# Kernel tuning notes

Measured on AMD Instinct MI355X. Metric: run time of the kernel, lower is better.

The kernel has to match this reference:

```python
import jax, jax.numpy as jnp
import numpy as np

N = 50000
E = 800000
NEG_SLOPE = 0.2
BN_EPS = 1e-5


def _gat_conv(x, src, dst, W, a_src, a_dst, bias, heads, out_ch, concat):
    # Linear projection per head: [N, heads, out_ch]
    h = (x @ W).reshape(-1, heads, out_ch)
    # Per-node attention terms alpha_src/alpha_dst: [N, heads]
    al_s = (h * a_src[None]).sum(-1)
    al_d = (h * a_dst[None]).sum(-1)
    # Edge logits with LeakyReLU: [E, heads]
    logits = jax.nn.leaky_relu(al_s[src] + al_d[dst], NEG_SLOPE)
    # Segment (scatter) softmax over edges grouped by destination node
    m = jax.ops.segment_max(logits, dst, num_segments=N)
    e = jnp.exp(logits - m[dst])
    s = jax.ops.segment_sum(e, dst, num_segments=N)
    alpha = e / (s[dst] + 1e-16)                      # [E, heads]
    # Weighted message aggregation: scatter-add to destinations
    msg = h[src] * alpha[:, :, None]                  # [E, heads, out_ch]
    out = jax.ops.segment_sum(msg, dst, num_segments=N)  # [N, heads, out_ch]
    out = out.reshape(-1, heads * out_ch) if concat else out.mean(axis=1)
    return out + bias


def _bn_eval(x, gamma, beta, mean, var):
    return (x - mean) * jax.lax.rsqrt(var + BN_EPS) * gamma + beta


def setup_inputs() -> dict:
    key = jax.random.key(0)
    ks = jax.random.split(key, 12)
    in_ch, hid, heads, out_cls = 128, 64, 2, 40
    return {
        "x": jax.random.normal(ks[0], (N, in_ch), jnp.float32),
        "edge_index": jax.random.randint(ks[1], (2, E), 0, N, jnp.int32),
        "W1": jax.random.normal(ks[2], (in_ch, heads * hid), jnp.float32) * 0.1,
        "a1_src": jax.random.normal(ks[3], (heads, hid), jnp.float32) * 0.1,
        "a1_dst": jax.random.normal(ks[4], (heads, hid), jnp.float32) * 0.1,
        "b1": jnp.zeros((heads * hid,), jnp.float32),
        "bn1_gamma": jnp.ones((heads * hid,), jnp.float32),
        "bn1_beta": jnp.zeros((heads * hid,), jnp.float32),
        "bn1_mean": jax.random.normal(ks[5], (heads * hid,), jnp.float32) * 0.1,
        "bn1_var": jax.random.uniform(ks[6], (heads * hid,), jnp.float32, 0.5, 1.5),
        "W2": jax.random.normal(ks[7], (heads * hid, out_cls), jnp.float32) * 0.1,
        "a2_src": jax.random.normal(ks[8], (1, out_cls), jnp.float32) * 0.1,
        "a2_dst": jax.random.normal(ks[9], (1, out_cls), jnp.float32) * 0.1,
        "b2": jnp.zeros((out_cls,), jnp.float32),
    }


def reference(x, edge_index, W1, a1_src, a1_dst, b1, bn1_gamma, bn1_beta,
              bn1_mean, bn1_var, W2, a2_src, a2_dst, b2):
    # add self loops
    loops = jnp.arange(N, dtype=edge_index.dtype)
    src = jnp.concatenate([edge_index[0], loops])
    dst = jnp.concatenate([edge_index[1], loops])
    # layer 1: GATConv(heads=2, concat) -> BN(eval) -> ReLU (dropout is eval no-op)
    h = _gat_conv(x, src, dst, W1, a1_src, a1_dst, b1, heads=2, out_ch=64, concat=True)
    h = jax.nn.relu(_bn_eval(h, bn1_gamma, bn1_beta, bn1_mean, bn1_var))
    # output layer: GATConv(heads=1, concat=False)
    out = _gat_conv(h, src, dst, W2, a2_src, a2_dst, b2, heads=1, out_ch=40, concat=False)
    return jax.nn.log_softmax(out, axis=1)
```

## Files before the change

### kernel.cpp

```cpp
#include <hip/hip_runtime.h>
#include <hip/hip_bf16.h>

#define NEG_SLOPE 0.2f
#define BN_EPS 1e-5f

#define NBLK 256
#define COARSE_SHIFT 9
#define COARSE_NPB 512

__device__ __forceinline__ float wred_sum(float v) {
    #pragma unroll
    for (int m = 32; m > 0; m >>= 1) v += __shfl_xor(v, m);
    return v;
}
__device__ __forceinline__ float wred_max(float v) {
    #pragma unroll
    for (int m = 32; m > 0; m >>= 1) v = fmaxf(v, __shfl_xor(v, m));
    return v;
}
__device__ __forceinline__ int wred_isum(int v) {
    #pragma unroll
    for (int m = 32; m > 0; m >>= 1) v += __shfl_xor(v, m);
    return v;
}
__device__ __forceinline__ float xor16_sum(float v) {
    #pragma unroll
    for (int m = 1; m < 16; m <<= 1) v += __shfl_xor(v, m);
    return v;
}

__device__ __forceinline__ unsigned pack_bf16(float a, float b) {
    __hip_bfloat162 t;
    t.x = __float2bfloat16(a);
    t.y = __float2bfloat16(b);
    return *(unsigned*)&t;
}
__device__ __forceinline__ float2 unpack_bf16(unsigned u) {
    __hip_bfloat162 t = *(__hip_bfloat162*)&u;
    return {__bfloat162float(t.x), __bfloat162float(t.y)};
}

__device__ __forceinline__ unsigned enc_ord(float f) {
    unsigned u = __float_as_uint(f);
    return (u & 0x80000000u) ? ~u : (u | 0x80000000u);
}
__device__ __forceinline__ float dec_ord(unsigned e) {
    unsigned u = (e & 0x80000000u) ? (e ^ 0x80000000u) : ~e;
    return __uint_as_float(u);
}

__global__ __launch_bounds__(256) void part_hist(const int* __restrict__ ei, int E, int Et,
                                                 int chunk, int* __restrict__ hist, int nCoarse) {
    __shared__ int h[128];
    int b = blockIdx.x, t = threadIdx.x;
    if (t < 128) h[t] = 0;
    __syncthreads();
    int beg = b * chunk, end = min(beg + chunk, Et);
    for (int idx = beg + t; idx < end; idx += 256) {
        int d = (idx < E) ? ei[E + idx] : (idx - E);
        atomicAdd(&h[d >> COARSE_SHIFT], 1);
    }
    __syncthreads();
    if (t < nCoarse) hist[t * NBLK + b] = h[t];
}

__global__ __launch_bounds__(1024) void csr_mid(int* __restrict__ hist,
                                                int* __restrict__ cbase, int nCoarse) {
    __shared__ int ctot_s[128];
    __shared__ int scn[128];
    __shared__ int cb_s[129];
    int t = threadIdx.x;
    int wv = t >> 6, ln = t & 63;
    if (t < 128) ctot_s[t] = 0;
    __syncthreads();
    for (int c = wv; c < nCoarse; c += 16) {
        int idx = c * NBLK + 4 * ln;
        int4 v = *(int4*)&hist[idx];
        int s = wred_isum(v.x + v.y + v.z + v.w);
        if (ln == 0) ctot_s[c] = s;
    }
    __syncthreads();
    int v0 = 0;
    if (t < 128) { v0 = ctot_s[t]; scn[t] = v0; }
    __syncthreads();
    for (int off = 1; off < 128; off <<= 1) {
        int u = (t >= off && t < 128) ? scn[t - off] : 0;
        __syncthreads();
        if (t < 128) scn[t] += u;
        __syncthreads();
    }
    if (t < 128) cb_s[t] = scn[t] - v0;
    if (t == 127) cb_s[128] = scn[127];
    __syncthreads();
    if (t <= nCoarse) cbase[t] = cb_s[t];
    for (int c = wv; c < nCoarse; c += 16) {
        int base = cb_s[c];
        int idx = c * NBLK + 4 * ln;
        int4 v = *(int4*)&hist[idx];
        int sl = v.x + v.y + v.z + v.w;
        int inc = sl;
        #pragma unroll
        for (int off = 1; off < 64; off <<= 1) {
            int u = __shfl_up(inc, off);
            if (ln >= off) inc += u;
        }
        int exc = inc - sl + base;
        int4 o;
        o.x = exc;
        o.y = exc + v.x;
        o.z = exc + v.x + v.y;
        o.w = exc + v.x + v.y + v.z;
        *(int4*)&hist[idx] = o;
    }
}

__global__ __launch_bounds__(256) void part_scatter(const int* __restrict__ ei, int E, int Et,
                                                    int chunk, const int* __restrict__ hist,
                                                    unsigned* __restrict__ staged, int nCoarse) {
    __shared__ int cur[128];
    int b = blockIdx.x, t = threadIdx.x;
    if (t < nCoarse) cur[t] = hist[t * NBLK + b];
    __syncthreads();
    int beg = b * chunk, end = min(beg + chunk, Et);
    for (int idx = beg + t; idx < end; idx += 256) {
        int s, d;
        if (idx < E) { s = ei[idx]; d = ei[E + idx]; }
        else         { s = idx - E; d = idx - E; }
        int c = d >> COARSE_SHIFT;
        int pos = atomicAdd(&cur[c], 1);
        staged[pos] = ((unsigned)s << COARSE_SHIFT) | (unsigned)(d & (COARSE_NPB - 1));
    }
}

__global__ __launch_bounds__(512) void fine_place(const unsigned* __restrict__ staged,
                                                  const int* __restrict__ cbase,
                                                  int* __restrict__ offs,
                                                  int* __restrict__ csr, int Nn, int nCoarse) {
    __shared__ int hcnt[COARSE_NPB];
    __shared__ int scn[COARSE_NPB];
    int b = blockIdx.x, t = threadIdx.x;
    int node0 = b << COARSE_SHIFT;
    int nloc = min(COARSE_NPB, Nn - node0);
    hcnt[t] = 0;
    __syncthreads();
    int ebeg = cbase[b], eend = cbase[b + 1];
    for (int p = ebeg + t; p < eend; p += 512) {
        atomicAdd(&hcnt[staged[p] & (COARSE_NPB - 1)], 1);
    }
    __syncthreads();
    int val = hcnt[t];
    scn[t] = val;
    __syncthreads();
    for (int off = 1; off < COARSE_NPB; off <<= 1) {
        int u = (t >= off) ? scn[t - off] : 0;
        __syncthreads();
        scn[t] += u;
        __syncthreads();
    }
    int exc = ebeg + scn[t] - val;
    if (t < nloc) offs[node0 + t] = exc;
    if (b == nCoarse - 1 && t == 0) offs[Nn] = eend;
    hcnt[t] = exc;
    __syncthreads();
    for (int p = ebeg + t; p < eend; p += 512) {
        unsigned v = staged[p];
        int pos = atomicAdd(&hcnt[v & (COARSE_NPB - 1)], 1);
        csr[pos] = (int)(v >> COARSE_SHIFT);
    }
}

__global__ __launch_bounds__(256) void gemm1_tiled(const float* __restrict__ x,
                                                   const float* __restrict__ W,
                                                   const float* __restrict__ a1s,
                                                   const float* __restrict__ a1d,
                                                   unsigned* __restrict__ h1b,
                                                   float* __restrict__ als,
                                                   float* __restrict__ ald, int Nn) {
    __shared__ float Ast[32][132];
    __shared__ float Bs[32][132];
    int t  = threadIdx.x;
    int tx = t & 15;
    int ty = t >> 4;
    int br = blockIdx.x * 128;

    float acc[8][8];
    #pragma unroll
    for (int i = 0; i < 8; ++i)
        #pragma unroll
        for (int j = 0; j < 8; ++j) acc[i][j] = 0.f;

    int k4   = t & 7;
    int rowA = t >> 3;

    for (int k0 = 0; k0 < 128; k0 += 32) {
        #pragma unroll
        for (int i = 0; i < 4; ++i) {
            int r  = rowA + 32 * i;
            int gr = min(br + r, Nn - 1);
            float4 v = *(const float4*)(x + (size_t)gr * 128 + k0 + 4 * k4);
            Ast[4 * k4 + 0][r] = v.x; Ast[4 * k4 + 1][r] = v.y;
            Ast[4 * k4 + 2][r] = v.z; Ast[4 * k4 + 3][r] = v.w;
        }
        #pragma unroll
        for (int i = 0; i < 4; ++i) {
            int f  = t + 256 * i;
            int kk = f >> 5, c4 = f & 31;
            *(float4*)&Bs[kk][4 * c4] = *(const float4*)(W + (size_t)(k0 + kk) * 128 + 4 * c4);
        }
        __syncthreads();
        #pragma unroll 8
        for (int kk = 0; kk < 32; ++kk) {
            float4 a0 = *(const float4*)&Ast[kk][8 * ty];
            float4 a1 = *(const float4*)&Ast[kk][8 * ty + 4];
            float4 b0 = *(const float4*)&Bs[kk][8 * tx];
            float4 b1 = *(const float4*)&Bs[kk][8 * tx + 4];
            float av[8] = {a0.x, a0.y, a0.z, a0.w, a1.x, a1.y, a1.z, a1.w};
            float bv[8] = {b0.x, b0.y, b0.z, b0.w, b1.x, b1.y, b1.z, b1.w};
            #pragma unroll
            for (int i = 0; i < 8; ++i)
                #pragma unroll
                for (int j = 0; j < 8; ++j) acc[i][j] += av[i] * bv[j];
        }
        __syncthreads();
    }

    float a_s[8], a_d[8];
    #pragma unroll
    for (int j = 0; j < 8; ++j) { a_s[j] = a1s[8 * tx + j]; a_d[j] = a1d[8 * tx + j]; }
    bool h0 = (tx < 8);

    #pragma unroll
    for (int i = 0; i < 8; ++i) {
        int r = br + 8 * ty + i;
        if (r < Nn) {
            uint4 pk;
            pk.x = pack_bf16(acc[i][0], acc[i][1]);
            pk.y = pack_bf16(acc[i][2], acc[i][3]);
            pk.z = pack_bf16(acc[i][4], acc[i][5]);
            pk.w = pack_bf16(acc[i][6], acc[i][7]);
            *(uint4*)(h1b + (size_t)r * 64 + 4 * tx) = pk;
        }
        float ps = 0.f, pd = 0.f;
        #pragma unroll
        for (int j = 0; j < 8; ++j) { ps += acc[i][j] * a_s[j]; pd += acc[i][j] * a_d[j]; }
        float s0 = xor16_sum(h0 ? ps : 0.f);
        float s1 = xor16_sum(h0 ? 0.f : ps);
        float d0 = xor16_sum(h0 ? pd : 0.f);
        float d1 = xor16_sum(h0 ? 0.f : pd);
        if (tx == 0 && r < Nn) {
            als[r * 2] = s0; als[r * 2 + 1] = s1;
            ald[r * 2] = d0; ald[r * 2 + 1] = d1;
        }
    }
}

template <int H>
__global__ __launch_bounds__(256) void almax_kernel(const float* __restrict__ als,
                                                    unsigned* __restrict__ gmax, int off, int Nn,
                                                    const float* __restrict__ b1,
                                                    const float* __restrict__ g1,
                                                    const float* __restrict__ be1,
                                                    const float* __restrict__ mn1,
                                                    const float* __restrict__ vr1,
                                                    float* __restrict__ bnscale,
                                                    float* __restrict__ bnshift) {
    __shared__ float red[4][H];
    int t = threadIdx.x;
    if (bnscale && blockIdx.x == 0 && t < 128) {
        float sc = rsqrtf(vr1[t] + BN_EPS) * g1[t];
        bnscale[t] = sc;
        bnshift[t] = be1[t] + (b1[t] - mn1[t]) * sc;
    }
    float m[H];
    #pragma unroll
    for (int h = 0; h < H; ++h) m[h] = -1e30f;
    for (int n = blockIdx.x * 256 + t; n < Nn; n += gridDim.x * 256) {
        #pragma unroll
        for (int h = 0; h < H; ++h) m[h] = fmaxf(m[h], als[n * H + h]);
    }
    #pragma unroll
    for (int h = 0; h < H; ++h) m[h] = wred_max(m[h]);
    int wid = t >> 6;
    if ((t & 63) == 0) {
        #pragma unroll
        for (int h = 0; h < H; ++h) red[wid][h] = m[h];
    }
    __syncthreads();
    if (t == 0) {
        #pragma unroll
        for (int h = 0; h < H; ++h) {
            float mm = fmaxf(fmaxf(red[0][h], red[1][h]), fmaxf(red[2][h], red[3][h]));
            atomicMax(&gmax[off + h], enc_ord(mm));
        }
    }
}

__global__ __launch_bounds__(256) void softagg1_kernel(const int* __restrict__ offs, const int* __restrict__ csr,
                            const unsigned* __restrict__ h1b,
                            const float* __restrict__ als, const float* __restrict__ ald,
                            const unsigned* __restrict__ gmax,
                            const float* __restrict__ bnscale, const float* __restrict__ bnshift,
                            unsigned* __restrict__ hbnb, int Nn) {
    __shared__ int   sh_s[4][4][16];
    __shared__ float sh_e[4][4][2][16];
    int wid = threadIdx.x >> 6, lane = threadIdx.x & 63;
    int g = lane >> 4;
    int l = lane & 15;
    int head = l >> 3;
    int n = blockIdx.x * 16 + wid * 4 + g;
    if (n >= Nn) return;
    int b = offs[n], e = offs[n + 1];
    float2 aldn = *(const float2*)(ald + (size_t)n * 2);
    float bd0 = dec_ord(gmax[0]) + aldn.x; bd0 = (bd0 > 0.f) ? bd0 : NEG_SLOPE * bd0;
    float bd1 = dec_ord(gmax[1]) + aldn.y; bd1 = (bd1 > 0.f) ? bd1 : NEG_SLOPE * bd1;

    float acc[8];
    #pragma unroll
    for (int j = 0; j < 8; ++j) acc[j] = 0.f;
    float den0 = 0.f, den1 = 0.f;

    for (int base = b; base < e; base += 16) {
        int cnt = min(16, e - base);
        int   s1 = 0;
        float e0r = 0.f, e1r = 0.f;
        if (l < cnt) {
            s1 = csr[base + l];
            float2 as = *(const float2*)(als + (size_t)s1 * 2);
            float l0 = as.x + aldn.x; l0 = (l0 > 0.f) ? l0 : NEG_SLOPE * l0;
            float l1 = as.y + aldn.y; l1 = (l1 > 0.f) ? l1 : NEG_SLOPE * l1;
            e0r = __expf(l0 - bd0);
            e1r = __expf(l1 - bd1);
            den0 += e0r; den1 += e1r;
        }
        sh_s[wid][g][l]    = s1;
        sh_e[wid][g][0][l] = e0r;
        sh_e[wid][g][1][l] = e1r;
        int i = 0;
        for (; i + 1 < cnt; i += 2) {
            int   sA  = sh_s[wid][g][i];
            int   sB  = sh_s[wid][g][i + 1];
            float evA = sh_e[wid][g][head][i];
            float evB = sh_e[wid][g][head][i + 1];
            uint4 vA = *(const uint4*)(h1b + (size_t)sA * 64 + 4 * l);
            uint4 vB = *(const uint4*)(h1b + (size_t)sB * 64 + 4 * l);
            float2 f;
            f = unpack_bf16(vA.x); acc[0] += f.x * evA; acc[1] += f.y * evA;
            f = unpack_bf16(vA.y); acc[2] += f.x * evA; acc[3] += f.y * evA;
            f = unpack_bf16(vA.z); acc[4] += f.x * evA; acc[5] += f.y * evA;
            f = unpack_bf16(vA.w); acc[6] += f.x * evA; acc[7] += f.y * evA;
            f = unpack_bf16(vB.x); acc[0] += f.x * evB; acc[1] += f.y * evB;
            f = unpack_bf16(vB.y); acc[2] += f.x * evB; acc[3] += f.y * evB;
            f = unpack_bf16(vB.z); acc[4] += f.x * evB; acc[5] += f.y * evB;
            f = unpack_bf16(vB.w); acc[6] += f.x * evB; acc[7] += f.y * evB;
        }
        if (i < cnt) {
            int   s  = sh_s[wid][g][i];
            float ev = sh_e[wid][g][head][i];
            uint4 v = *(const uint4*)(h1b + (size_t)s * 64 + 4 * l);
            float2 f;
            f = unpack_bf16(v.x); acc[0] += f.x * ev; acc[1] += f.y * ev;
            f = unpack_bf16(v.y); acc[2] += f.x * ev; acc[3] += f.y * ev;
            f = unpack_bf16(v.z); acc[4] += f.x * ev; acc[5] += f.y * ev;
            f = unpack_bf16(v.w); acc[6] += f.x * ev; acc[7] += f.y * ev;
        }
    }
    #pragma unroll
    for (int m = 1; m < 16; m <<= 1) {
        den0 += __shfl_xor(den0, m);
        den1 += __shfl_xor(den1, m);
    }
    float inv = 1.f / ((head ? den1 : den0) + 1e-16f);
    int c = 8 * l;
    float4 sa = *(const float4*)(bnscale + c), sb = *(const float4*)(bnscale + c + 4);
    float4 ha = *(const float4*)(bnshift + c), hb = *(const float4*)(bnshift + c + 4);
    float o0 = fmaxf(acc[0] * inv * sa.x + ha.x, 0.f);
    float o1 = fmaxf(acc[1] * inv * sa.y + ha.y, 0.f);
    float o2 = fmaxf(acc[2] * inv * sa.z + ha.z, 0.f);
    float o3 = fmaxf(acc[3] * inv * sa.w + ha.w, 0.f);
    float o4 = fmaxf(acc[4] * inv * sb.x + hb.x, 0.f);
    float o5 = fmaxf(acc[5] * inv * sb.y + hb.y, 0.f);
    float o6 = fmaxf(acc[6] * inv * sb.z + hb.z, 0.f);
    float o7 = fmaxf(acc[7] * inv * sb.w + hb.w, 0.f);
    uint4 pk = {pack_bf16(o0, o1), pack_bf16(o2, o3), pack_bf16(o4, o5), pack_bf16(o6, o7)};
    *(uint4*)(hbnb + (size_t)n * 64 + 4 * l) = pk;
}

__global__ __launch_bounds__(256) void gemm2_tiled(const unsigned* __restrict__ hbnb,
                                                   const float* __restrict__ W2,
                                                   const float* __restrict__ a2s,
                                                   const float* __restrict__ a2d,
                                                   unsigned* __restrict__ h2b,
                                                   float* __restrict__ als, float* __restrict__ ald,
                                                   int Nn) {
    __shared__ float Ast[32][132];
    __shared__ float Bs[32][68];
    int t  = threadIdx.x;
    int tx = t & 15;
    int ty = t >> 4;
    int br = blockIdx.x * 128;

    float as4[4], ad4[4];
    #pragma unroll
    for (int j = 0; j < 4; ++j) {
        int c = 4 * tx + j;
        as4[j] = (c < 40) ? a2s[c] : 0.f;
        ad4[j] = (c < 40) ? a2d[c] : 0.f;
    }

    float acc[8][4];
    #pragma unroll
    for (int i = 0; i < 8; ++i)
        #pragma unroll
        for (int j = 0; j < 4; ++j) acc[i][j] = 0.f;

    int k4   = t & 7;
    int rowA = t >> 3;

    for (int k0 = 0; k0 < 128; k0 += 32) {
        #pragma unroll
        for (int i = 0; i < 4; ++i) {
            int r  = rowA + 32 * i;
            int gr = min(br + r, Nn - 1);
            uint2 v2 = *(const uint2*)(hbnb + (size_t)gr * 64 + (k0 >> 1) + 2 * k4);
            float2 f0 = unpack_bf16(v2.x), f1 = unpack_bf16(v2.y);
            Ast[4 * k4 + 0][r] = f0.x; Ast[4 * k4 + 1][r] = f0.y;
            Ast[4 * k4 + 2][r] = f1.x; Ast[4 * k4 + 3][r] = f1.y;
        }
        #pragma unroll
        for (int i = 0; i < 2; ++i) {
            int f  = t + 256 * i;
            int kk = f >> 4, c4 = f & 15;
            float4 v = {0.f, 0.f, 0.f, 0.f};
            if (c4 < 10) v = *(const float4*)(W2 + (size_t)(k0 + kk) * 40 + 4 * c4);
            *(float4*)&Bs[kk][4 * c4] = v;
        }
        __syncthreads();
        #pragma unroll 8
        for (int kk = 0; kk < 32; ++kk) {
            float4 a0 = *(const float4*)&Ast[kk][8 * ty];
            float4 a1 = *(const float4*)&Ast[kk][8 * ty + 4];
            float4 b0 = *(const float4*)&Bs[kk][4 * tx];
            float av[8] = {a0.x, a0.y, a0.z, a0.w, a1.x, a1.y, a1.z, a1.w};
            #pragma unroll
            for (int i = 0; i < 8; ++i) {
                acc[i][0] += av[i] * b0.x; acc[i][1] += av[i] * b0.y;
                acc[i][2] += av[i] * b0.z; acc[i][3] += av[i] * b0.w;
            }
        }
        __syncthreads();
    }

    #pragma unroll
    for (int i = 0; i < 8; ++i) {
        int r = br + 8 * ty + i;
        if (r < Nn && tx < 10) {
            uint2 pk = {pack_bf16(acc[i][0], acc[i][1]), pack_bf16(acc[i][2], acc[i][3])};
            *(uint2*)(h2b + (size_t)r * 20 + 2 * tx) = pk;
        }
        float ps = acc[i][0] * as4[0] + acc[i][1] * as4[1] + acc[i][2] * as4[2] + acc[i][3] * as4[3];
        float pd = acc[i][0] * ad4[0] + acc[i][1] * ad4[1] + acc[i][2] * ad4[2] + acc[i][3] * ad4[3];
        float sS = xor16_sum(ps);
        float sD = xor16_sum(pd);
        if (tx == 0 && r < Nn) { als[r] = sS; ald[r] = sD; }
    }
}

__global__ __launch_bounds__(256) void softagg2_kernel(const int* __restrict__ offs, const int* __restrict__ csr,
                            const unsigned* __restrict__ h2b,
                            const float* __restrict__ als, const float* __restrict__ ald,
                            const unsigned* __restrict__ gmax,
                            const float* __restrict__ b2,
                            float* __restrict__ out, int Nn) {
    __shared__ int   sh_s[4][8][8];
    __shared__ float sh_ev[4][8][8];
    int wid = threadIdx.x >> 6, lane = threadIdx.x & 63;
    int g = lane >> 3;
    int l = lane & 7;
    int n = blockIdx.x * 32 + wid * 8 + g;
    if (n >= Nn) return;
    int b = offs[n], e = offs[n + 1];
    float aldn = ald[n];
    float bound = dec_ord(gmax[2]) + aldn;
    bound = (bound > 0.f) ? bound : NEG_SLOPE * bound;

    float acc[8];
    #pragma unroll
    for (int j = 0; j < 8; ++j) acc[j] = 0.f;
    float den = 0.f;

    for (int base = b; base < e; base += 8) {
        int cnt = min(8, e - base);
        int   s1 = 0;
        float evr = 0.f;
        if (l < cnt) {
            s1 = csr[base + l];
            float lv = als[s1] + aldn;
            lv = (lv > 0.f) ? lv : NEG_SLOPE * lv;
            evr = __expf(lv - bound);
            den += evr;
        }
        sh_s[wid][g][l]  = s1;
        sh_ev[wid][g][l] = evr;
        if (l < 5) {
            int i = 0;
            for (; i + 1 < cnt; i += 2) {
                int   sA  = sh_s[wid][g][i];
                int   sB  = sh_s[wid][g][i + 1];
                float evA = sh_ev[wid][g][i];
                float evB = sh_ev[wid][g][i + 1];
                uint4 vA = *(const uint4*)(h2b + (size_t)sA * 20 + 4 * l);
                uint4 vB = *(const uint4*)(h2b + (size_t)sB * 20 + 4 * l);
                float2 f;
                f = unpack_bf16(vA.x); acc[0] += f.x * evA; acc[1] += f.y * evA;
                f = unpack_bf16(vA.y); acc[2] += f.x * evA; acc[3] += f.y * evA;
                f = unpack_bf16(vA.z); acc[4] += f.x * evA; acc[5] += f.y * evA;
                f = unpack_bf16(vA.w); acc[6] += f.x * evA; acc[7] += f.y * evA;
                f = unpack_bf16(vB.x); acc[0] += f.x * evB; acc[1] += f.y * evB;
                f = unpack_bf16(vB.y); acc[2] += f.x * evB; acc[3] += f.y * evB;
                f = unpack_bf16(vB.z); acc[4] += f.x * evB; acc[5] += f.y * evB;
                f = unpack_bf16(vB.w); acc[6] += f.x * evB; acc[7] += f.y * evB;
            }
            if (i < cnt) {
                int   s  = sh_s[wid][g][i];
                float ev = sh_ev[wid][g][i];
                uint4 v = *(const uint4*)(h2b + (size_t)s * 20 + 4 * l);
                float2 f;
                f = unpack_bf16(v.x); acc[0] += f.x * ev; acc[1] += f.y * ev;
                f = unpack_bf16(v.y); acc[2] += f.x * ev; acc[3] += f.y * ev;
                f = unpack_bf16(v.z); acc[4] += f.x * ev; acc[5] += f.y * ev;
                f = unpack_bf16(v.w); acc[6] += f.x * ev; acc[7] += f.y * ev;
            }
        }
    }
    #pragma unroll
    for (int m = 1; m < 8; m <<= 1) den += __shfl_xor(den, m);
    float inv = 1.f / (den + 1e-16f);
    bool valid = (l < 5);
    float vv[8];
    float lmax = -1e30f;
    if (valid) {
        int c = 8 * l;
        #pragma unroll
        for (int j = 0; j < 8; ++j) {
            vv[j] = acc[j] * inv + b2[c + j];
            lmax = fmaxf(lmax, vv[j]);
        }
    }
    float m = lmax;
    #pragma unroll
    for (int mm = 1; mm < 8; mm <<= 1) m = fmaxf(m, __shfl_xor(m, mm));
    float es = 0.f;
    if (valid) {
        #pragma unroll
        for (int j = 0; j < 8; ++j) es += __expf(vv[j] - m);
    }
    #pragma unroll
    for (int mm = 1; mm < 8; mm <<= 1) es += __shfl_xor(es, mm);
    float lse = m + logf(es);
    if (valid) {
        float4 oa = {vv[0] - lse, vv[1] - lse, vv[2] - lse, vv[3] - lse};
        float4 ob = {vv[4] - lse, vv[5] - lse, vv[6] - lse, vv[7] - lse};
        *(float4*)(out + (size_t)n * 40 + 8 * l)     = oa;
        *(float4*)(out + (size_t)n * 40 + 8 * l + 4) = ob;
    }
}

extern "C" void kernel_launch(void* const* d_in, const int* in_sizes, int n_in,
                              void* d_out, int out_size, void* d_ws, size_t ws_size,
                              hipStream_t stream) {
    const float* x    = (const float*)d_in[0];
    const int*   ei   = (const int*)d_in[1];
    const float* W1   = (const float*)d_in[2];
    const float* a1s  = (const float*)d_in[3];
    const float* a1d  = (const float*)d_in[4];
    const float* b1   = (const float*)d_in[5];
    const float* g1   = (const float*)d_in[6];
    const float* be1  = (const float*)d_in[7];
    const float* mn1  = (const float*)d_in[8];
    const float* vr1  = (const float*)d_in[9];
    const float* W2   = (const float*)d_in[10];
    const float* a2s  = (const float*)d_in[11];
    const float* a2d  = (const float*)d_in[12];
    const float* b2   = (const float*)d_in[13];
    float* out = (float*)d_out;

    const int N  = in_sizes[0] / 128;
    const int E  = in_sizes[1] / 2;
    const int Et = E + N;
    const int nCoarse = (N + COARSE_NPB - 1) >> COARSE_SHIFT;
    const int chunk   = (Et + NBLK - 1) / NBLK;

    char* p = (char*)d_ws;
    auto alloc = [&](size_t bytes) -> void* {
        void* r = (void*)p;
        p += (bytes + 255) & ~(size_t)255;
        return r;
    };
    int*      hist   = (int*)alloc((size_t)nCoarse * NBLK * 4);
    int*      cbase  = (int*)alloc((size_t)(nCoarse + 1) * 4);
    int*      offs   = (int*)alloc((size_t)(N + 1) * 4);
    unsigned* staged = (unsigned*)alloc((size_t)Et * 4);
    int*      csr    = (int*)alloc((size_t)Et * 4);
    unsigned* h1b    = (unsigned*)alloc((size_t)N * 64 * 4);
    float*    al1sv  = (float*)alloc((size_t)N * 2 * 4);
    float*    al1dv  = (float*)alloc((size_t)N * 2 * 4);
    unsigned* hbnb   = (unsigned*)alloc((size_t)N * 64 * 4);
    unsigned* h2b    = (unsigned*)alloc((size_t)N * 20 * 4);
    float*    al2sv  = (float*)alloc((size_t)N * 4);
    float*    al2dv  = (float*)alloc((size_t)N * 4);
    unsigned* gmax   = (unsigned*)alloc(4 * 4);
    float*    bnscale= (float*)alloc(128 * 4);
    float*    bnshift= (float*)alloc(128 * 4);
    (void)ws_size;

    hipMemsetAsync(gmax, 0, 16, stream);

    part_hist<<<NBLK, 256, 0, stream>>>(ei, E, Et, chunk, hist, nCoarse);
    csr_mid<<<1, 1024, 0, stream>>>(hist, cbase, nCoarse);
    part_scatter<<<NBLK, 256, 0, stream>>>(ei, E, Et, chunk, hist, staged, nCoarse);
    fine_place<<<nCoarse, 512, 0, stream>>>(staged, cbase, offs, csr, N, nCoarse);

    gemm1_tiled<<<(N + 127) / 128, 256, 0, stream>>>(x, W1, a1s, a1d, h1b, al1sv, al1dv, N);
    almax_kernel<2><<<64, 256, 0, stream>>>(al1sv, gmax, 0, N, b1, g1, be1, mn1, vr1, bnscale, bnshift);
    softagg1_kernel<<<(N + 15) / 16, 256, 0, stream>>>(offs, csr, h1b, al1sv, al1dv, gmax,
                                                       bnscale, bnshift, hbnb, N);

    gemm2_tiled<<<(N + 127) / 128, 256, 0, stream>>>(hbnb, W2, a2s, a2d, h2b, al2sv, al2dv, N);
    almax_kernel<1><<<64, 256, 0, stream>>>(al2sv, gmax, 2, N, nullptr, nullptr, nullptr, nullptr,
                                            nullptr, nullptr, nullptr);
    softagg2_kernel<<<(N + 31) / 32, 256, 0, stream>>>(offs, csr, h2b, al2sv, al2dv, gmax, b2, out, N);
}
```

Before: 241.3 us.

## Use bf16 MFMA for first-layer projection GEMM and fold gmax reset into histogram

Replaces the FP32 register-tiled SIMT GEMM for layer 1 with a bf16 MFMA 16x16x32 kernel. W is converted into per-lane bf16 fragments in shared memory, x rows are converted to bf16 on load, and accumulators are staged through LDS so h1 is written as packed bf16 rows. It also removes the separate memset launch by zeroing gmax inside part_hist. Inputs to the projection now lose precision to bf16, and each block re-gathers and converts all of W with uncoalesced loads.

```diff
diff --git a/kernel.cpp b/kernel.cpp
--- a/kernel.cpp
+++ b/kernel.cpp
@@ -7,6 +7,9 @@
 #define NBLK 256
 #define COARSE_SHIFT 9
 #define COARSE_NPB 512
+
+typedef __attribute__((ext_vector_type(8))) short s8v;
+typedef __attribute__((ext_vector_type(4))) float f4v;
 
 __device__ __forceinline__ float wred_sum(float v) {
     #pragma unroll
@@ -39,6 +42,10 @@
     __hip_bfloat162 t = *(__hip_bfloat162*)&u;
     return {__bfloat162float(t.x), __bfloat162float(t.y)};
 }
+__device__ __forceinline__ short bf16s(float f) {
+    __hip_bfloat16 h = __float2bfloat16(f);
+    return *(short*)&h;
+}
 
 __device__ __forceinline__ unsigned enc_ord(float f) {
     unsigned u = __float_as_uint(f);
@@ -50,9 +57,11 @@
 }
 
 __global__ __launch_bounds__(256) void part_hist(const int* __restrict__ ei, int E, int Et,
-                                                 int chunk, int* __restrict__ hist, int nCoarse) {
+                                                 int chunk, int* __restrict__ hist, int nCoarse,
+                                                 unsigned* __restrict__ gmax) {
     __shared__ int h[128];
     int b = blockIdx.x, t = threadIdx.x;
+    if (b == 0 && t < 4) gmax[t] = 0u;
     if (t < 128) h[t] = 0;
     __syncthreads();
     int beg = b * chunk, end = min(beg + chunk, Et);
@@ -169,87 +178,103 @@
     }
 }
 
-__global__ __launch_bounds__(256) void gemm1_tiled(const float* __restrict__ x,
-                                                   const float* __restrict__ W,
-                                                   const float* __restrict__ a1s,
-                                                   const float* __restrict__ a1d,
-                                                   unsigned* __restrict__ h1b,
-                                                   float* __restrict__ als,
-                                                   float* __restrict__ ald, int Nn) {
-    __shared__ float Ast[32][132];
-    __shared__ float Bs[32][132];
-    int t  = threadIdx.x;
-    int tx = t & 15;
-    int ty = t >> 4;
-    int br = blockIdx.x * 128;
-
-    float acc[8][8];
-    #pragma unroll
-    for (int i = 0; i < 8; ++i)
-        #pragma unroll
-        for (int j = 0; j < 8; ++j) acc[i][j] = 0.f;
-
-    int k4   = t & 7;
-    int rowA = t >> 3;
-
-    for (int k0 = 0; k0 < 128; k0 += 32) {
+__global__ __launch_bounds__(256) void gemm1_mfma(const float* __restrict__ x,
+                                                  const float* __restrict__ W,
+                                                  const float* __restrict__ a1s,
+                                                  const float* __restrict__ a1d,
+                                                  unsigned* __restrict__ h1b,
+                                                  float* __restrict__ als,
+                                                  float* __restrict__ ald, int Nn) {
+    __shared__ __align__(16) char smem[33792];
+    short* fragtab = (short*)smem;
+    float* lout    = (float*)smem;
+
+    int t = threadIdx.x;
+    int br = blockIdx.x * 64;
+
+    #pragma unroll
+    for (int i = 0; i < 8; ++i) {
+        int s   = t + 256 * i;
+        int grp = s >> 6;
+        int ls  = s & 63;
+        int ct = grp >> 2, kc = grp & 3;
+        int nn = ls & 15, quad = ls >> 4;
+        int kb = kc * 32 + quad * 8;
+        int cc = ct * 16 + nn;
+        #pragma unroll
+        for (int j = 0; j < 8; ++j)
+            fragtab[s * 8 + j] = bf16s(W[(size_t)(kb + j) * 128 + cc]);
+    }
+    __syncthreads();
+
+    int w    = t >> 6;
+    int lane = t & 63;
+    int nn   = lane & 15;
+    int quad = lane >> 4;
+    int rowbase = br + w * 16;
+    int arow = min(rowbase + nn, Nn - 1);
+    const float* xr = x + (size_t)arow * 128;
+
+    f4v acc[8];
+    #pragma unroll
+    for (int ct = 0; ct < 8; ++ct) acc[ct] = (f4v){0.f, 0.f, 0.f, 0.f};
+
+    #pragma unroll
+    for (int kc = 0; kc < 4; ++kc) {
+        float4 v0 = *(const float4*)(xr + kc * 32 + quad * 8);
+        float4 v1 = *(const float4*)(xr + kc * 32 + quad * 8 + 4);
+        union { s8v s; uint4 u; } A;
+        A.u.x = pack_bf16(v0.x, v0.y); A.u.y = pack_bf16(v0.z, v0.w);
+        A.u.z = pack_bf16(v1.x, v1.y); A.u.w = pack_bf16(v1.z, v1.w);
+        #pragma unroll
+        for (int ct = 0; ct < 8; ++ct) {
+            s8v B = *(s8v*)(fragtab + (size_t)((ct * 4 + kc) * 64 + lane) * 8);
+            acc[ct] = __builtin_amdgcn_mfma_f32_16x16x32_bf16(A.s, B, acc[ct], 0, 0, 0);
+        }
+    }
+
+    float s_c[8], d_c[8];
+    #pragma unroll
+    for (int ct = 0; ct < 8; ++ct) {
+        s_c[ct] = a1s[ct * 16 + nn];
+        d_c[ct] = a1d[ct * 16 + nn];
+    }
+    #pragma unroll
+    for (int reg = 0; reg < 4; ++reg) {
+        float ps0 = 0.f, pd0 = 0.f, ps1 = 0.f, pd1 = 0.f;
+        #pragma unroll
+        for (int ct = 0; ct < 4; ++ct) { ps0 += acc[ct][reg] * s_c[ct]; pd0 += acc[ct][reg] * d_c[ct]; }
+        #pragma unroll
+        for (int ct = 4; ct < 8; ++ct) { ps1 += acc[ct][reg] * s_c[ct]; pd1 += acc[ct][reg] * d_c[ct]; }
+        ps0 = xor16_sum(ps0); pd0 = xor16_sum(pd0);
+        ps1 = xor16_sum(ps1); pd1 = xor16_sum(pd1);
+        int r = rowbase + quad * 4 + reg;
+        if (nn == 0 && r < Nn) {
+            als[(size_t)r * 2]     = ps0;
+            als[(size_t)r * 2 + 1] = ps1;
+            ald[(size_t)r * 2]     = pd0;
+            ald[(size_t)r * 2 + 1] = pd1;
+        }
+    }
+
+    __syncthreads();
+    #pragma unroll
+    for (int ct = 0; ct < 8; ++ct)
+        #pragma unroll
+        for (int reg = 0; reg < 4; ++reg)
+            lout[w * 2112 + (quad * 4 + reg) * 132 + ct * 16 + nn] = acc[ct][reg];
+    int row_l = lane >> 2;
+    int ch    = lane & 3;
+    int r = rowbase + row_l;
+    if (r < Nn) {
+        const float* src = lout + w * 2112 + row_l * 132 + ch * 32;
         #pragma unroll
         for (int i = 0; i < 4; ++i) {
-            int r  = rowA + 32 * i;
-            int gr = min(br + r, Nn - 1);
-            float4 v = *(const float4*)(x + (size_t)gr * 128 + k0 + 4 * k4);
-            Ast[4 * k4 + 0][r] = v.x; Ast[4 * k4 + 1][r] = v.y;
-            Ast[4 * k4 + 2][r] = v.z; Ast[4 * k4 + 3][r] = v.w;
-        }
-        #pragma unroll
-        for (int i = 0; i < 4; ++i) {
-            int f  = t + 256 * i;
-            int kk = f >> 5, c4 = f & 31;
-            *(float4*)&Bs[kk][4 * c4] = *(const float4*)(W + (size_t)(k0 + kk) * 128 + 4 * c4);
-        }
-        __syncthreads();
-        #pragma unroll 8
-        for (int kk = 0; kk < 32; ++kk) {
-            float4 a0 = *(const float4*)&Ast[kk][8 * ty];
-            float4 a1 = *(const float4*)&Ast[kk][8 * ty + 4];
-            float4 b0 = *(const float4*)&Bs[kk][8 * tx];
-            float4 b1 = *(const float4*)&Bs[kk][8 * tx + 4];
-            float av[8] = {a0.x, a0.y, a0.z, a0.w, a1.x, a1.y, a1.z, a1.w};
-            float bv[8] = {b0.x, b0.y, b0.z, b0.w, b1.x, b1.y, b1.z, b1.w};
-            #pragma unroll
-            for (int i = 0; i < 8; ++i)
-                #pragma unroll
-                for (int j = 0; j < 8; ++j) acc[i][j] += av[i] * bv[j];
-        }
-        __syncthreads();
-    }
-
-    float a_s[8], a_d[8];
-    #pragma unroll
-    for (int j = 0; j < 8; ++j) { a_s[j] = a1s[8 * tx + j]; a_d[j] = a1d[8 * tx + j]; }
-    bool h0 = (tx < 8);
-
-    #pragma unroll
-    for (int i = 0; i < 8; ++i) {
-        int r = br + 8 * ty + i;
-        if (r < Nn) {
-            uint4 pk;
-            pk.x = pack_bf16(acc[i][0], acc[i][1]);
-            pk.y = pack_bf16(acc[i][2], acc[i][3]);
-            pk.z = pack_bf16(acc[i][4], acc[i][5]);
-            pk.w = pack_bf16(acc[i][6], acc[i][7]);
-            *(uint4*)(h1b + (size_t)r * 64 + 4 * tx) = pk;
-        }
-        float ps = 0.f, pd = 0.f;
-        #pragma unroll
-        for (int j = 0; j < 8; ++j) { ps += acc[i][j] * a_s[j]; pd += acc[i][j] * a_d[j]; }
-        float s0 = xor16_sum(h0 ? ps : 0.f);
-        float s1 = xor16_sum(h0 ? 0.f : ps);
-        float d0 = xor16_sum(h0 ? pd : 0.f);
-        float d1 = xor16_sum(h0 ? 0.f : pd);
-        if (tx == 0 && r < Nn) {
-            als[r * 2] = s0; als[r * 2 + 1] = s1;
-            ald[r * 2] = d0; ald[r * 2 + 1] = d1;
+            uint4 pk = {pack_bf16(src[8 * i + 0], src[8 * i + 1]),
+                        pack_bf16(src[8 * i + 2], src[8 * i + 3]),
+                        pack_bf16(src[8 * i + 4], src[8 * i + 5]),
+                        pack_bf16(src[8 * i + 6], src[8 * i + 7])};
+            *(uint4*)(h1b + (size_t)r * 64 + ch * 16 + i * 4) = pk;
         }
     }
 }
@@ -613,14 +638,12 @@
     float*    bnshift= (float*)alloc(128 * 4);
     (void)ws_size;
 
-    hipMemsetAsync(gmax, 0, 16, stream);
-
-    part_hist<<<NBLK, 256, 0, stream>>>(ei, E, Et, chunk, hist, nCoarse);
+    part_hist<<<NBLK, 256, 0, stream>>>(ei, E, Et, chunk, hist, nCoarse, gmax);
     csr_mid<<<1, 1024, 0, stream>>>(hist, cbase, nCoarse);
     part_scatter<<<NBLK, 256, 0, stream>>>(ei, E, Et, chunk, hist, staged, nCoarse);
     fine_place<<<nCoarse, 512, 0, stream>>>(staged, cbase, offs, csr, N, nCoarse);
 
-    gemm1_tiled<<<(N + 127) / 128, 256, 0, stream>>>(x, W1, a1s, a1d, h1b, al1sv, al1dv, N);
+    gemm1_mfma<<<(N + 63) / 64, 256, 0, stream>>>(x, W1, a1s, a1d, h1b, al1sv, al1dv, N);
     almax_kernel<2><<<64, 256, 0, stream>>>(al1sv, gmax, 0, N, b1, g1, be1, mn1, vr1, bnscale, bnshift);
     softagg1_kernel<<<(N + 15) / 16, 256, 0, stream>>>(offs, csr, h1b, al1sv, al1dv, gmax,
                                                        bnscale, bnshift, hbnb, N);
```

Measured after the change: 225.2 us. 6.7% less time.
